# Performance work log

Hardware: AMD Instinct MI355X
Metric: run time of the kernel (lower is better)

The kernel has to match this reference:

```python
import jax, jax.numpy as jnp
import numpy as np
from jax import lax

E = 32          # num_experts
H = 1024        # hidden_size
I = 512         # expert intermediate_size
IS = 2048       # shared expert intermediate_size
G = 8           # n_group
TOPK_GROUP = 4
TOP_K = 8
SCALE = 2.5     # routed_scaling_factor
T = 1024        # tokens


def setup_inputs() -> dict:
    key = jax.random.key(0)
    ks = jax.random.split(key, 9)
    s = 0.02
    return {
        "hidden_states": jax.random.normal(ks[0], (T, H), jnp.float32),
        "gate_w": jax.random.normal(ks[1], (E, H), jnp.float32) * s,
        "e_bias": jax.random.normal(ks[2], (E,), jnp.float32) * 0.1,
        "w_gate": jax.random.normal(ks[3], (E, H, I), jnp.float32) * s,
        "w_up": jax.random.normal(ks[4], (E, H, I), jnp.float32) * s,
        "w_down": jax.random.normal(ks[5], (E, I, H), jnp.float32) * s,
        "ws_gate": jax.random.normal(ks[6], (H, IS), jnp.float32) * s,
        "ws_up": jax.random.normal(ks[7], (H, IS), jnp.float32) * s,
        "ws_down": jax.random.normal(ks[8], (IS, H), jnp.float32) * s,
    }


def _routing_combine(logits, e_bias):
    # Deepseekv3RoutingImpl.noaux_tc (non-fused reference path)
    scores = jax.nn.sigmoid(logits)                    # [T, E]
    swb = scores + e_bias                              # [T, E]
    swb_g = swb.reshape(-1, G, E // G)                 # [T, G, E/G]
    group_scores = lax.top_k(swb_g, 2)[0].sum(-1)      # sum of top-2 per group
    _, gidx = lax.top_k(group_scores, TOPK_GROUP)      # [T, TOPK_GROUP]
    gmask = jax.nn.one_hot(gidx, G, dtype=swb.dtype).sum(1)   # [T, G]
    smask = jnp.repeat(gmask, E // G, axis=-1)         # [T, E]
    _, tidx = lax.top_k(swb * smask, TOP_K)            # [T, TOP_K]
    emask = jax.nn.one_hot(tidx, E, dtype=scores.dtype).sum(1)
    sc = scores * emask
    combine = sc / (sc.sum(-1, keepdims=True) + 1e-20) * SCALE
    return combine, tidx


def reference(hidden_states, gate_w, e_bias, w_gate, w_up, w_down, ws_gate, ws_up, ws_down):
    x = hidden_states
    # gate: fp32 logits
    logits = x.astype(jnp.float32) @ gate_w.T          # [T, E]
    combine, _ = _routing_combine(logits, e_bias)
    # routed experts (FusedMoE math): per-expert gated MLP, combined by routing weights
    h1 = jnp.einsum('th,ehi->tei', x, w_gate)          # [T, E, I]
    h2 = jnp.einsum('th,ehi->tei', x, w_up)
    act = jax.nn.silu(h1) * h2
    routed = jnp.einsum('tei,te,eih->th', act, combine.astype(x.dtype), w_down)
    # shared expert GatedMLP
    shared = (jax.nn.silu(x @ ws_gate) * (x @ ws_up)) @ ws_down
    return routed + shared
```

## Files before the change

### kernel.cpp

```cpp
#include <hip/hip_runtime.h>
#include <cstdint>
#include <cmath>

#define T_TOK 1024
#define H_DIM 1024
#define E_NUM 32
#define I_DIM 512
#define IS_DIM 2048
#define NCOL_R 16384
#define NCOL_T 18432
#define SCALE_F 2.5f
#define MAXTILES 96

typedef __bf16 bf16x8 __attribute__((ext_vector_type(8)));
typedef float f32x4 __attribute__((ext_vector_type(4)));

typedef __attribute__((address_space(3))) unsigned int lds_u32_t;
typedef __attribute__((address_space(1))) const unsigned int glb_u32_t;

__device__ __forceinline__ unsigned short f2b(float f) {
    union { float f; uint32_t u; } v; v.f = f;
    return (unsigned short)((v.u + 0x7FFFu + ((v.u >> 16) & 1u)) >> 16);
}

__device__ __forceinline__ uint32_t cvt2(float lo, float hi) {
    uint32_t r;
    asm("v_cvt_pk_bf16_f32 %0, %1, %2" : "=v"(r) : "v"(lo), "v"(hi));
    return r;
}

__device__ __forceinline__ void gll16(const unsigned short* g, unsigned short* l) {
    __builtin_amdgcn_global_load_lds((glb_u32_t*)g, (lds_u32_t*)l, 16, 0, 0);
}

__device__ __forceinline__ void routing_wave(const float* __restrict__ x,
                                             const float* __restrict__ gate_w,
                                             const float* __restrict__ e_bias,
                                             float* __restrict__ combine,
                                             int* __restrict__ topk, int t) {
    int l = threadIdx.x & 63;
    int e = l & 31, half = l >> 5;
    const float4* xr = reinterpret_cast<const float4*>(x + (size_t)t * H_DIM + half * 512);
    const float4* wr = reinterpret_cast<const float4*>(gate_w + (size_t)e * H_DIM + half * 512);
    float s = 0.f;
#pragma unroll 8
    for (int j = 0; j < 128; j++) {
        float4 a = xr[j], b = wr[j];
        s += a.x * b.x + a.y * b.y + a.z * b.z + a.w * b.w;
    }
    s += __shfl_xor(s, 32);
    float sg = 1.f / (1.f + expf(-s));
    float swb = sg + e_bias[e];
    float v1 = __shfl_xor(swb, 1), v2 = __shfl_xor(swb, 2), v3 = __shfl_xor(swb, 3);
    float hi01 = fmaxf(swb, v1), lo01 = fminf(swb, v1);
    float hi23 = fmaxf(v2, v3),  lo23 = fminf(v2, v3);
    float gs = fmaxf(hi01, hi23) + fmaxf(fminf(hi01, hi23), fmaxf(lo01, lo23));
    int g = e >> 2;
    int grank = 0;
#pragma unroll
    for (int gg = 0; gg < 8; gg++) {
        float og = __shfl(gs, gg * 4);
        grank += ((og > gs) || (og == gs && gg < g)) ? 1 : 0;
    }
    bool gsel = grank < 4;
    float candv = gsel ? swb : 0.0f;
    int erank = 0;
#pragma unroll
    for (int ee = 0; ee < 32; ee++) {
        float oc = __shfl(candv, ee);
        erank += ((oc > candv) || (oc == candv && ee < e)) ? 1 : 0;
    }
    bool esel = (erank < 8) && (half == 0);
    unsigned long long m = __ballot(esel);
    int idx = __popcll(m & ((1ull << l) - 1ull));
    if (esel) topk[t * 8 + idx] = e;
    float r = esel ? sg : 0.f;
#pragma unroll
    for (int off = 1; off < 64; off <<= 1) r += __shfl_xor(r, off);
    float inv = SCALE_F / (r + 1e-20f);
    if (half == 0) combine[t * E_NUM + e] = esel ? sg * inv : 0.0f;
}

__global__ __launch_bounds__(256)
void prep1_kernel(const float* __restrict__ x, const float* __restrict__ gate_w,
                  const float* __restrict__ e_bias,
                  unsigned short* __restrict__ xb, float* __restrict__ combine,
                  int* __restrict__ topk) {
    int b = blockIdx.x;
    if (b < 256) {
        int t = b * 4 + (threadIdx.x >> 6);
        routing_wave(x, gate_w, e_bias, combine, topk, t);
        return;
    }
    int bb = b - 256;
#pragma unroll
    for (int p = 0; p < 4; p++) {
        int i = bb * 1024 + p * 256 + threadIdx.x;
        float4 v = reinterpret_cast<const float4*>(x)[i];
        uint2 o;
        o.x = cvt2(v.x, v.y);
        o.y = cvt2(v.z, v.w);
        reinterpret_cast<uint2*>(xb)[i] = o;
    }
}

__global__ __launch_bounds__(1024)
void listbuild_kernel(const int* __restrict__ topk, int* __restrict__ meta,
                      int* __restrict__ pair_token, int* __restrict__ slot_of) {
    __shared__ int cnt[E_NUM], start[E_NUM], fill[E_NUM];
    int t = threadIdx.x;
    if (t < E_NUM) cnt[t] = 0;
    __syncthreads();
    int ids[8];
#pragma unroll
    for (int r = 0; r < 8; r++) {
        ids[r] = topk[t * 8 + r];
        atomicAdd(&cnt[ids[r]], 1);
    }
    __syncthreads();
    if (t == 0) {
        int acc = 0;
        for (int e = 0; e < E_NUM; e++) {
            int nt = (cnt[e] + 127) >> 7;
            start[e] = acc * 128;
            fill[e] = 0;
            for (int j = 0; j < nt; j++) meta[1 + acc + j] = e;
            acc += nt;
        }
        meta[0] = acc;
    }
    __syncthreads();
    for (int i = t; i < MAXTILES * 128; i += 1024) pair_token[i] = 0;
    __syncthreads();
#pragma unroll
    for (int r = 0; r < 8; r++) {
        int e = ids[r];
        int s = start[e] + atomicAdd(&fill[e], 1);
        pair_token[s] = t;
        slot_of[t * 8 + r] = s;
    }
}

__global__ __launch_bounds__(256, 2)
void gateup_fused(const unsigned short* __restrict__ xb,
                  const float* __restrict__ w_gate,
                  const float* __restrict__ w_up,
                  const float* __restrict__ ws_gate,
                  const float* __restrict__ ws_up,
                  const float* __restrict__ combine,
                  const int* __restrict__ pair_token,
                  const int* __restrict__ meta,
                  unsigned short* __restrict__ act_s,
                  unsigned short* __restrict__ act_sh) {
    int b = blockIdx.x;
    bool routed = b < 384;
    int tid = threadIdx.x, lane = tid & 63, w = tid >> 6;
    int wr = w >> 1, wc = w & 1;
    __shared__ __align__(16) unsigned short lA[2][128 * 32];
    __shared__ __align__(16) unsigned short lBg[2][128 * 40];
    __shared__ __align__(16) unsigned short lBu[2][128 * 40];

    int srow = w * 32 + (lane >> 2);
    int schunk = (lane & 3) * 8;
    int aoff = (w * 32) * 32;

    const unsigned short *gA0, *gA1;
    const float *gBg, *gBu;
    int bstride;
    int e = 0, slot0 = 0, row0 = 0, ci0 = 0;
    if (routed) {
        int tile = b >> 2;
        if (tile >= meta[0]) return;
        e = meta[1 + tile];
        ci0 = (b & 3) * 128;
        slot0 = tile * 128;
        int tok0 = pair_token[slot0 + srow];
        int tok1 = pair_token[slot0 + srow + 16];
        gA0 = xb + (size_t)tok0 * H_DIM + schunk;
        gA1 = xb + (size_t)tok1 * H_DIM + schunk;
        gBg = w_gate + (size_t)e * H_DIM * I_DIM + ci0;
        gBu = w_up   + (size_t)e * H_DIM * I_DIM + ci0;
        bstride = I_DIM;
    } else {
        int bb = b - 384;
        row0 = (bb >> 4) * 128;
        ci0 = (bb & 15) * 128;
        gA0 = xb + (size_t)(row0 + srow) * H_DIM + schunk;
        gA1 = gA0 + 16 * H_DIM;
        gBg = ws_gate + ci0;
        gBu = ws_up + ci0;
        bstride = IS_DIM;
    }
    int bcol = tid & 127, khalf = tid >> 7;

    f32x4 accg[4][4], accu[4][4];
#pragma unroll
    for (int i = 0; i < 4; i++)
#pragma unroll
        for (int j = 0; j < 4; j++)
#pragma unroll
            for (int r = 0; r < 4; r++) { accg[i][j][r] = 0.f; accu[i][j][r] = 0.f; }

    float rg[16], ru[16];

#define GU_LOADB(KK)                                                    \
    do {                                                                \
        size_t kb = (size_t)((KK) * 32 + khalf * 16);                   \
        _Pragma("unroll")                                               \
        for (int j = 0; j < 16; j++) {                                  \
            rg[j] = gBg[(kb + j) * bstride + bcol];                     \
            ru[j] = gBu[(kb + j) * bstride + bcol];                     \
        }                                                               \
    } while (0)

#define GU_GLLA(KK, BSEL)                                               \
    do {                                                                \
        int _k0 = (KK) * 32;                                            \
        unsigned short* _a = &lA[BSEL][aoff];                           \
        gll16(gA0 + _k0, _a);                                           \
        gll16(gA1 + _k0, _a + 16 * 32);                                 \
    } while (0)

#define GU_WRB(BSEL)                                                    \
    do {                                                                \
        uint4 u;                                                        \
        unsigned short* dg = &lBg[BSEL][bcol * 40 + khalf * 16];        \
        u.x = cvt2(rg[0], rg[1]);  u.y = cvt2(rg[2], rg[3]);            \
        u.z = cvt2(rg[4], rg[5]);  u.w = cvt2(rg[6], rg[7]);            \
        *reinterpret_cast<uint4*>(dg) = u;                              \
        u.x = cvt2(rg[8], rg[9]);  u.y = cvt2(rg[10], rg[11]);          \
        u.z = cvt2(rg[12], rg[13]); u.w = cvt2(rg[14], rg[15]);         \
        *reinterpret_cast<uint4*>(dg + 8) = u;                          \
        unsigned short* du = &lBu[BSEL][bcol * 40 + khalf * 16];        \
        u.x = cvt2(ru[0], ru[1]);  u.y = cvt2(ru[2], ru[3]);            \
        u.z = cvt2(ru[4], ru[5]);  u.w = cvt2(ru[6], ru[7]);            \
        *reinterpret_cast<uint4*>(du) = u;                              \
        u.x = cvt2(ru[8], ru[9]);  u.y = cvt2(ru[10], ru[11]);          \
        u.z = cvt2(ru[12], ru[13]); u.w = cvt2(ru[14], ru[15]);         \
        *reinterpret_cast<uint4*>(du + 8) = u;                          \
    } while (0)

    GU_GLLA(0, 0);
    GU_LOADB(0);
    __syncthreads();
    GU_WRB(0);
    __syncthreads();
    for (int kk = 0; kk < 32; kk++) {
        int cur = kk & 1;
        if (kk < 31) { GU_GLLA(kk + 1, cur ^ 1); GU_LOADB(kk + 1); }
        bf16x8 af[4], bgf[4], buf2[4];
#pragma unroll
        for (int mi = 0; mi < 4; mi++)
            af[mi] = *reinterpret_cast<const bf16x8*>(
                &lA[cur][(wr * 64 + mi * 16 + (lane & 15)) * 32 + (lane >> 4) * 8]);
#pragma unroll
        for (int ni = 0; ni < 4; ni++) {
            int nn = (wc * 64 + ni * 16 + (lane & 15)) * 40 + (lane >> 4) * 8;
            bgf[ni] = *reinterpret_cast<const bf16x8*>(&lBg[cur][nn]);
            buf2[ni] = *reinterpret_cast<const bf16x8*>(&lBu[cur][nn]);
        }
#pragma unroll
        for (int mi = 0; mi < 4; mi++)
#pragma unroll
            for (int ni = 0; ni < 4; ni++) {
                accg[mi][ni] = __builtin_amdgcn_mfma_f32_16x16x32_bf16(af[mi], bgf[ni], accg[mi][ni], 0, 0, 0);
                accu[mi][ni] = __builtin_amdgcn_mfma_f32_16x16x32_bf16(af[mi], buf2[ni], accu[mi][ni], 0, 0, 0);
            }
        __syncthreads();
        if (kk < 31) {
            GU_WRB(cur ^ 1);
            __syncthreads();
        }
    }
#undef GU_LOADB
#undef GU_GLLA
#undef GU_WRB

    int q = lane >> 4, cl = lane & 15;
    if (routed) {
#pragma unroll
        for (int mi = 0; mi < 4; mi++) {
#pragma unroll
            for (int r = 0; r < 4; r++) {
                int row = wr * 64 + mi * 16 + q * 4 + r;
                int token = pair_token[slot0 + row];
                float s = combine[token * E_NUM + e];
#pragma unroll
                for (int ni = 0; ni < 4; ni++) {
                    float g = accg[mi][ni][r], u = accu[mi][ni][r];
                    float a = g / (1.f + expf(-g)) * u * s;
                    act_s[(size_t)(slot0 + row) * I_DIM + ci0 + wc * 64 + ni * 16 + cl] = f2b(a);
                }
            }
        }
    } else {
#pragma unroll
        for (int mi = 0; mi < 4; mi++) {
#pragma unroll
            for (int ni = 0; ni < 4; ni++) {
                int col = ci0 + wc * 64 + ni * 16 + cl;
#pragma unroll
                for (int r = 0; r < 4; r++) {
                    int row = row0 + wr * 64 + mi * 16 + q * 4 + r;
                    float g = accg[mi][ni][r], u = accu[mi][ni][r];
                    float a = g / (1.f + expf(-g)) * u;
                    act_sh[(size_t)row * IS_DIM + col] = f2b(a);
                }
            }
        }
    }
}

__global__ __launch_bounds__(256, 3)
void down_fused(const unsigned short* __restrict__ act_s,
                const float* __restrict__ w_down,
                const unsigned short* __restrict__ act_sh,
                const float* __restrict__ ws_down,
                const int* __restrict__ meta,
                float* __restrict__ pairpart,
                float* __restrict__ shpart) {
    int b = blockIdx.x;
    bool routed = b < 768;
    int tid = threadIdx.x, lane = tid & 63, w = tid >> 6;
    int wr = w >> 1, wc = w & 1;
    __shared__ __align__(16) unsigned short lA[2][128 * 32];
    __shared__ __align__(16) unsigned short lB[2][128 * 40];

    int srow = w * 32 + (lane >> 2);
    int schunk = (lane & 3) * 8;
    int aoff = (w * 32) * 32;

    const unsigned short* gA0;
    const float* gB;
    size_t ast;
    int kbase, n0, orow;
    float* outp;
    if (routed) {
        int tile = b >> 3;
        if (tile >= meta[0]) return;
        int e = meta[1 + tile];
        n0 = (b & 7) * 128;
        int slot0 = tile * 128;
        gA0 = act_s + (size_t)(slot0 + srow) * I_DIM + schunk;
        gB = w_down + (size_t)e * I_DIM * H_DIM + n0;
        ast = I_DIM; kbase = 0;
        outp = pairpart; orow = slot0;
    } else {
        int bb = b - 768;
        int mb = bb >> 5, nb = (bb >> 2) & 7, ks = bb & 3;
        int row0 = mb * 128;
        n0 = nb * 128;
        gA0 = act_sh + (size_t)(row0 + srow) * IS_DIM + schunk;
        gB = ws_down + n0;
        ast = IS_DIM; kbase = ks * 512;
        outp = shpart + ((size_t)ks << 20); orow = row0;
    }
    int bcol = tid & 127, khalf = tid >> 7;

    f32x4 acc[4][4];
#pragma unroll
    for (int i = 0; i < 4; i++)
#pragma unroll
        for (int j = 0; j < 4; j++)
#pragma unroll
            for (int r = 0; r < 4; r++) acc[i][j][r] = 0.f;

    float rb[16];

#define DN_LOADB(KK)                                                    \
    do {                                                                \
        size_t kb = (size_t)(kbase + (KK) * 32 + khalf * 16);           \
        _Pragma("unroll")                                               \
        for (int j = 0; j < 16; j++)                                    \
            rb[j] = gB[(kb + j) * H_DIM + bcol];                        \
    } while (0)

#define DN_GLLA(KK, BSEL)                                               \
    do {                                                                \
        size_t _k0 = (size_t)kbase + (size_t)(KK) * 32;                 \
        unsigned short* _a = &lA[BSEL][aoff];                           \
        gll16(gA0 + _k0, _a);                                           \
        gll16(gA0 + 16 * ast + _k0, _a + 16 * 32);                      \
    } while (0)

#define DN_WRB(BSEL)                                                    \
    do {                                                                \
        uint4 u;                                                        \
        unsigned short* d = &lB[BSEL][bcol * 40 + khalf * 16];          \
        u.x = cvt2(rb[0], rb[1]);  u.y = cvt2(rb[2], rb[3]);            \
        u.z = cvt2(rb[4], rb[5]);  u.w = cvt2(rb[6], rb[7]);            \
        *reinterpret_cast<uint4*>(d) = u;                               \
        u.x = cvt2(rb[8], rb[9]);  u.y = cvt2(rb[10], rb[11]);          \
        u.z = cvt2(rb[12], rb[13]); u.w = cvt2(rb[14], rb[15]);         \
        *reinterpret_cast<uint4*>(d + 8) = u;                           \
    } while (0)

    DN_GLLA(0, 0);
    DN_LOADB(0);
    __syncthreads();
    DN_WRB(0);
    __syncthreads();
    for (int kk = 0; kk < 16; kk++) {
        int cur = kk & 1;
        if (kk < 15) { DN_GLLA(kk + 1, cur ^ 1); DN_LOADB(kk + 1); }
        bf16x8 af[4], bf[4];
#pragma unroll
        for (int mi = 0; mi < 4; mi++)
            af[mi] = *reinterpret_cast<const bf16x8*>(
                &lA[cur][(wr * 64 + mi * 16 + (lane & 15)) * 32 + (lane >> 4) * 8]);
#pragma unroll
        for (int ni = 0; ni < 4; ni++)
            bf[ni] = *reinterpret_cast<const bf16x8*>(
                &lB[cur][(wc * 64 + ni * 16 + (lane & 15)) * 40 + (lane >> 4) * 8]);
#pragma unroll
        for (int mi = 0; mi < 4; mi++)
#pragma unroll
            for (int ni = 0; ni < 4; ni++)
                acc[mi][ni] = __builtin_amdgcn_mfma_f32_16x16x32_bf16(af[mi], bf[ni], acc[mi][ni], 0, 0, 0);
        __syncthreads();
        if (kk < 15) {
            DN_WRB(cur ^ 1);
            __syncthreads();
        }
    }
#undef DN_LOADB
#undef DN_GLLA
#undef DN_WRB

    int q = lane >> 4, cl = lane & 15;
#pragma unroll
    for (int mi = 0; mi < 4; mi++) {
#pragma unroll
        for (int ni = 0; ni < 4; ni++) {
            int col = n0 + wc * 64 + ni * 16 + cl;
#pragma unroll
            for (int r = 0; r < 4; r++) {
                int row = orow + wr * 64 + mi * 16 + q * 4 + r;
                outp[(size_t)row * H_DIM + col] = acc[mi][ni][r];
            }
        }
    }
}

__global__ void final_combine(const float* __restrict__ pairpart,
                              const float* __restrict__ shpart,
                              const int* __restrict__ slot_of,
                              float* __restrict__ out) {
    int t = blockIdx.x;
    int h = threadIdx.x * 4;
    float4 o = reinterpret_cast<const float4*>(shpart + (size_t)t * H_DIM + h)[0];
#pragma unroll
    for (int ks = 1; ks < 4; ks++) {
        float4 v = reinterpret_cast<const float4*>(shpart + ((size_t)ks << 20) + (size_t)t * H_DIM + h)[0];
        o.x += v.x; o.y += v.y; o.z += v.z; o.w += v.w;
    }
#pragma unroll
    for (int r = 0; r < 8; r++) {
        int s = slot_of[t * 8 + r];
        float4 v = reinterpret_cast<const float4*>(pairpart + (size_t)s * H_DIM + h)[0];
        o.x += v.x; o.y += v.y; o.z += v.z; o.w += v.w;
    }
    reinterpret_cast<float4*>(out + (size_t)t * H_DIM + h)[0] = o;
}


__global__ void cvt_x_kernel(const float* __restrict__ x, unsigned short* __restrict__ xb) {
    int i = blockIdx.x * 256 + threadIdx.x;
    float4 v = reinterpret_cast<const float4*>(x)[i];
    uint2 o;
    o.x = (uint32_t)f2b(v.x) | ((uint32_t)f2b(v.y) << 16);
    o.y = (uint32_t)f2b(v.z) | ((uint32_t)f2b(v.w) << 16);
    reinterpret_cast<uint2*>(xb)[i] = o;
}

__global__ void routing_kernel(const float* __restrict__ x,
                               const float* __restrict__ gate_w,
                               const float* __restrict__ e_bias,
                               float* __restrict__ combine,
                               int* __restrict__ topk) {
    int t = blockIdx.x;
    routing_wave(x, gate_w, e_bias, combine, topk, t);
}

__global__ __launch_bounds__(256, 2)
void gateup_kernel(const unsigned short* __restrict__ xb,
                   const float* __restrict__ w_gate,
                   const float* __restrict__ w_up,
                   const float* __restrict__ ws_gate,
                   const float* __restrict__ ws_up,
                   const float* __restrict__ combine,
                   unsigned short* __restrict__ act) {
    int mb = blockIdx.x, cb = blockIdx.y;
    int row0 = mb * 128, c0 = cb * 128;
    const float *bg, *bu;
    int bstride, eidx;
    if (c0 < NCOL_R) {
        int e = c0 >> 9, ci = c0 & 511;
        bg = w_gate + (size_t)e * H_DIM * I_DIM + ci;
        bu = w_up   + (size_t)e * H_DIM * I_DIM + ci;
        bstride = I_DIM; eidx = e;
    } else {
        int ci = c0 - NCOL_R;
        bg = ws_gate + ci; bu = ws_up + ci;
        bstride = IS_DIM; eidx = -1;
    }
    __shared__ __align__(16) unsigned short lA[128*32];
    __shared__ __align__(16) unsigned short lBg[128*32];
    __shared__ __align__(16) unsigned short lBu[128*32];
    int tid = threadIdx.x, lane = tid & 63, w = tid >> 6;
    int wr = w >> 1, wc = w & 1;
    f32x4 accg[4][4], accu[4][4];
#pragma unroll
    for (int i = 0; i < 4; i++)
#pragma unroll
        for (int j = 0; j < 4; j++)
#pragma unroll
            for (int r = 0; r < 4; r++) { accg[i][j][r] = 0.f; accu[i][j][r] = 0.f; }
    int ar = tid >> 2, ak = (tid & 3) * 8;
    int bn = tid & 127, bkg = (tid >> 7) * 16;
    for (int kk = 0; kk < H_DIM / 32; kk++) {
        int k0 = kk * 32;
        __syncthreads();
        *reinterpret_cast<uint4*>(&lA[ar*32 + ak]) =
            *reinterpret_cast<const uint4*>(xb + (size_t)(row0 + ar) * H_DIM + k0 + ak);
        *reinterpret_cast<uint4*>(&lA[(ar+64)*32 + ak]) =
            *reinterpret_cast<const uint4*>(xb + (size_t)(row0 + ar + 64) * H_DIM + k0 + ak);
#pragma unroll
        for (int p = 0; p < 4; p++) {
            int kb = bkg + p * 4;
            const float* pg = bg + (size_t)(k0 + kb) * bstride + bn;
            uint2 dg;
            dg.x = (uint32_t)f2b(pg[0])         | ((uint32_t)f2b(pg[bstride])   << 16);
            dg.y = (uint32_t)f2b(pg[2*bstride]) | ((uint32_t)f2b(pg[3*bstride]) << 16);
            *reinterpret_cast<uint2*>(&lBg[bn*32 + kb]) = dg;
            const float* pu = bu + (size_t)(k0 + kb) * bstride + bn;
            uint2 du;
            du.x = (uint32_t)f2b(pu[0])         | ((uint32_t)f2b(pu[bstride])   << 16);
            du.y = (uint32_t)f2b(pu[2*bstride]) | ((uint32_t)f2b(pu[3*bstride]) << 16);
            *reinterpret_cast<uint2*>(&lBu[bn*32 + kb]) = du;
        }
        __syncthreads();
        bf16x8 af[4], bgf[4], buf2[4];
#pragma unroll
        for (int mi = 0; mi < 4; mi++)
            af[mi] = *reinterpret_cast<const bf16x8*>(&lA[(wr*64 + mi*16 + (lane & 15))*32 + (lane >> 4)*8]);
#pragma unroll
        for (int ni = 0; ni < 4; ni++) {
            int nn = (wc*64 + ni*16 + (lane & 15))*32 + (lane >> 4)*8;
            bgf[ni]  = *reinterpret_cast<const bf16x8*>(&lBg[nn]);
            buf2[ni] = *reinterpret_cast<const bf16x8*>(&lBu[nn]);
        }
#pragma unroll
        for (int mi = 0; mi < 4; mi++)
#pragma unroll
            for (int ni = 0; ni < 4; ni++) {
                accg[mi][ni] = __builtin_amdgcn_mfma_f32_16x16x32_bf16(af[mi], bgf[ni],  accg[mi][ni], 0, 0, 0);
                accu[mi][ni] = __builtin_amdgcn_mfma_f32_16x16x32_bf16(af[mi], buf2[ni], accu[mi][ni], 0, 0, 0);
            }
    }
    int q = lane >> 4, cl = lane & 15;
#pragma unroll
    for (int mi = 0; mi < 4; mi++) {
#pragma unroll
        for (int ni = 0; ni < 4; ni++) {
            int colg = c0 + wc*64 + ni*16 + cl;
#pragma unroll
            for (int r = 0; r < 4; r++) {
                int row = row0 + wr*64 + mi*16 + q*4 + r;
                float g = accg[mi][ni][r], u = accu[mi][ni][r];
                float a = g / (1.f + expf(-g)) * u;
                float s = (eidx >= 0) ? combine[row * E_NUM + eidx] : 1.0f;
                act[(size_t)row * NCOL_T + colg] = f2b(a * s);
            }
        }
    }
}

__global__ __launch_bounds__(256, 2)
void down_kernel(const unsigned short* __restrict__ act,
                 const float* __restrict__ w_down,
                 const float* __restrict__ ws_down,
                 float* __restrict__ partials) {
    int mb = blockIdx.x, nb = blockIdx.y, ks = blockIdx.z;
    int row0 = mb * 128, n0 = nb * 128;
    __shared__ __align__(16) unsigned short lA[128*32];
    __shared__ __align__(16) unsigned short lB[128*32];
    int tid = threadIdx.x, lane = tid & 63, w = tid >> 6;
    int wr = w >> 1, wc = w & 1;
    f32x4 acc[4][4];
#pragma unroll
    for (int i = 0; i < 4; i++)
#pragma unroll
        for (int j = 0; j < 4; j++)
#pragma unroll
            for (int r = 0; r < 4; r++) acc[i][j][r] = 0.f;
    int ar = tid >> 2, ak = (tid & 3) * 8;
    int bn = tid & 127, bkg = (tid >> 7) * 16;
    for (int kk = 0; kk < 144; kk++) {
        int k0 = ks * 4608 + kk * 32;
        const float* bb = (k0 < NCOL_R) ? (w_down + (size_t)k0 * H_DIM)
                                        : (ws_down + (size_t)(k0 - NCOL_R) * H_DIM);
        __syncthreads();
        *reinterpret_cast<uint4*>(&lA[ar*32 + ak]) =
            *reinterpret_cast<const uint4*>(act + (size_t)(row0 + ar) * NCOL_T + k0 + ak);
        *reinterpret_cast<uint4*>(&lA[(ar+64)*32 + ak]) =
            *reinterpret_cast<const uint4*>(act + (size_t)(row0 + ar + 64) * NCOL_T + k0 + ak);
#pragma unroll
        for (int p = 0; p < 4; p++) {
            int kb = bkg + p * 4;
            const float* pb = bb + (size_t)kb * H_DIM + n0 + bn;
            uint2 d;
            d.x = (uint32_t)f2b(pb[0])       | ((uint32_t)f2b(pb[H_DIM])   << 16);
            d.y = (uint32_t)f2b(pb[2*H_DIM]) | ((uint32_t)f2b(pb[3*H_DIM]) << 16);
            *reinterpret_cast<uint2*>(&lB[bn*32 + kb]) = d;
        }
        __syncthreads();
        bf16x8 af[4], bf[4];
#pragma unroll
        for (int mi = 0; mi < 4; mi++)
            af[mi] = *reinterpret_cast<const bf16x8*>(&lA[(wr*64 + mi*16 + (lane & 15))*32 + (lane >> 4)*8]);
#pragma unroll
        for (int ni = 0; ni < 4; ni++)
            bf[ni] = *reinterpret_cast<const bf16x8*>(&lB[(wc*64 + ni*16 + (lane & 15))*32 + (lane >> 4)*8]);
#pragma unroll
        for (int mi = 0; mi < 4; mi++)
#pragma unroll
            for (int ni = 0; ni < 4; ni++)
                acc[mi][ni] = __builtin_amdgcn_mfma_f32_16x16x32_bf16(af[mi], bf[ni], acc[mi][ni], 0, 0, 0);
    }
    float* pout = partials + ((size_t)ks << 20);
    int q = lane >> 4, cl = lane & 15;
#pragma unroll
    for (int mi = 0; mi < 4; mi++) {
#pragma unroll
        for (int ni = 0; ni < 4; ni++) {
            int col = n0 + wc*64 + ni*16 + cl;
#pragma unroll
            for (int r = 0; r < 4; r++) {
                int row = row0 + wr*64 + mi*16 + q*4 + r;
                pout[(size_t)row * H_DIM + col] = acc[mi][ni][r];
            }
        }
    }
}

__global__ void reduce_kernel(const float* __restrict__ p, float* __restrict__ out) {
    int i = blockIdx.x * 256 + threadIdx.x;
    float4 a = reinterpret_cast<const float4*>(p)[i];
    float4 b = reinterpret_cast<const float4*>(p + (size_t)1048576)[i];
    float4 c = reinterpret_cast<const float4*>(p + (size_t)2097152)[i];
    float4 d = reinterpret_cast<const float4*>(p + (size_t)3145728)[i];
    float4 o;
    o.x = a.x + b.x + c.x + d.x;
    o.y = a.y + b.y + c.y + d.y;
    o.z = a.z + b.z + c.z + d.z;
    o.w = a.w + b.w + c.w + d.w;
    reinterpret_cast<float4*>(out)[i] = o;
}

extern "C" void kernel_launch(void* const* d_in, const int* in_sizes, int n_in,
                              void* d_out, int out_size, void* d_ws, size_t ws_size,
                              hipStream_t stream) {
    const float* x       = (const float*)d_in[0];
    const float* gate_w  = (const float*)d_in[1];
    const float* e_bias  = (const float*)d_in[2];
    const float* w_gate  = (const float*)d_in[3];
    const float* w_up    = (const float*)d_in[4];
    const float* w_down  = (const float*)d_in[5];
    const float* ws_gate = (const float*)d_in[6];
    const float* ws_up   = (const float*)d_in[7];
    const float* ws_down = (const float*)d_in[8];
    float* out = (float*)d_out;

    char* ws = (char*)d_ws;
    bool fast = ws_size >= 170000384ull;

    if (fast) {
        float* combine      = (float*)(ws);
        int*   topk         = (int*)(ws + 131072);
        int*   meta         = (int*)(ws + 163840);
        int*   pair_token   = (int*)(ws + 164352);
        int*   slot_of      = (int*)(ws + 213504);
        unsigned short* xb  = (unsigned short*)(ws + 262144);
        unsigned short* act_s  = (unsigned short*)(ws + 2359296);
        unsigned short* act_sh = (unsigned short*)(ws + 14942208);
        float* pairpart     = (float*)(ws + 19136512);
        float* shpart       = (float*)(ws + 69468160);

        prep1_kernel<<<512, 256, 0, stream>>>(x, gate_w, e_bias, xb, combine, topk);
        listbuild_kernel<<<1, 1024, 0, stream>>>(topk, meta, pair_token, slot_of);
        gateup_fused<<<512, 256, 0, stream>>>(xb, w_gate, w_up, ws_gate, ws_up,
                                              combine, pair_token, meta, act_s, act_sh);
        down_fused<<<1024, 256, 0, stream>>>(act_s, w_down, act_sh, ws_down, meta,
                                             pairpart, shpart);
        final_combine<<<1024, 256, 0, stream>>>(pairpart, shpart, slot_of, out);
    } else {
        float* combine     = (float*)(ws);
        int*   topk        = (int*)(ws + 131072);
        unsigned short* xb = (unsigned short*)(ws + 262144);
        unsigned short* act= (unsigned short*)(ws + 2359296);
        float* partials    = (float*)(ws + 40108032);

        cvt_x_kernel<<<1024, 256, 0, stream>>>(x, xb);
        routing_kernel<<<1024, 64, 0, stream>>>(x, gate_w, e_bias, combine, topk);
        gateup_kernel<<<dim3(8, 144), 256, 0, stream>>>(xb, w_gate, w_up, ws_gate, ws_up, combine, act);
        down_kernel<<<dim3(8, 8, 4), 256, 0, stream>>>(act, w_down, ws_down, partials);
        reduce_kernel<<<1024, 256, 0, stream>>>(partials, out);
    }
}
```

Measured before the change: 337.8 us.

## Halve gate/up column tile, single-buffer B in LDS, vectorize weight loads

The gate/up kernel's N tile drops from 128 to 64 columns, so the grid doubles to 1024 blocks and accumulator registers are halved. Occupancy hints rise to 4 blocks per CU in both GEMM kernels. The B-operand LDS buffers become single-buffered. Global fp32 weight loads become float2 reads, with each thread writing transposed bf16 pairs for two adjacent columns. The aim is more resident waves and fewer load instructions, at the cost of re-reading each A tile twice as often and less reuse per block.

```diff
diff --git a/kernel.cpp b/kernel.cpp
--- a/kernel.cpp
+++ b/kernel.cpp
@@ -141,7 +141,7 @@
     }
 }
 
-__global__ __launch_bounds__(256, 2)
+__global__ __launch_bounds__(256, 4)
 void gateup_fused(const unsigned short* __restrict__ xb,
                   const float* __restrict__ w_gate,
                   const float* __restrict__ w_up,
@@ -153,26 +153,28 @@
                   unsigned short* __restrict__ act_s,
                   unsigned short* __restrict__ act_sh) {
     int b = blockIdx.x;
-    bool routed = b < 384;
+    bool routed = b < 768;
     int tid = threadIdx.x, lane = tid & 63, w = tid >> 6;
     int wr = w >> 1, wc = w & 1;
     __shared__ __align__(16) unsigned short lA[2][128 * 32];
-    __shared__ __align__(16) unsigned short lBg[2][128 * 40];
-    __shared__ __align__(16) unsigned short lBu[2][128 * 40];
+    __shared__ __align__(16) unsigned short lBg[64 * 40];
+    __shared__ __align__(16) unsigned short lBu[64 * 40];
 
     int srow = w * 32 + (lane >> 2);
     int schunk = (lane & 3) * 8;
     int aoff = (w * 32) * 32;
+    int nc = (tid & 31) * 2;
+    int kg = tid >> 5;
 
     const unsigned short *gA0, *gA1;
     const float *gBg, *gBu;
     int bstride;
     int e = 0, slot0 = 0, row0 = 0, ci0 = 0;
     if (routed) {
-        int tile = b >> 2;
+        int tile = b >> 3;
         if (tile >= meta[0]) return;
         e = meta[1 + tile];
-        ci0 = (b & 3) * 128;
+        ci0 = (b & 7) * 64;
         slot0 = tile * 128;
         int tok0 = pair_token[slot0 + srow];
         int tok1 = pair_token[slot0 + srow + 16];
@@ -182,34 +184,33 @@
         gBu = w_up   + (size_t)e * H_DIM * I_DIM + ci0;
         bstride = I_DIM;
     } else {
-        int bb = b - 384;
-        row0 = (bb >> 4) * 128;
-        ci0 = (bb & 15) * 128;
+        int bb = b - 768;
+        row0 = (bb >> 5) * 128;
+        ci0 = (bb & 31) * 64;
         gA0 = xb + (size_t)(row0 + srow) * H_DIM + schunk;
         gA1 = gA0 + 16 * H_DIM;
         gBg = ws_gate + ci0;
         gBu = ws_up + ci0;
         bstride = IS_DIM;
     }
-    int bcol = tid & 127, khalf = tid >> 7;
-
-    f32x4 accg[4][4], accu[4][4];
+
+    f32x4 accg[4][2], accu[4][2];
 #pragma unroll
     for (int i = 0; i < 4; i++)
 #pragma unroll
-        for (int j = 0; j < 4; j++)
+        for (int j = 0; j < 2; j++)
 #pragma unroll
             for (int r = 0; r < 4; r++) { accg[i][j][r] = 0.f; accu[i][j][r] = 0.f; }
 
-    float rg[16], ru[16];
+    float2 vg[4], vu[4];
 
 #define GU_LOADB(KK)                                                    \
     do {                                                                \
-        size_t kb = (size_t)((KK) * 32 + khalf * 16);                   \
+        size_t kb = (size_t)((KK) * 32 + kg * 4);                       \
         _Pragma("unroll")                                               \
-        for (int j = 0; j < 16; j++) {                                  \
-            rg[j] = gBg[(kb + j) * bstride + bcol];                     \
-            ru[j] = gBu[(kb + j) * bstride + bcol];                     \
+        for (int j = 0; j < 4; j++) {                                   \
+            vg[j] = *reinterpret_cast<const float2*>(&gBg[(kb + j) * bstride + nc]); \
+            vu[j] = *reinterpret_cast<const float2*>(&gBu[(kb + j) * bstride + nc]); \
         }                                                               \
     } while (0)
 
@@ -221,54 +222,48 @@
         gll16(gA1 + _k0, _a + 16 * 32);                                 \
     } while (0)
 
-#define GU_WRB(BSEL)                                                    \
+#define GU_WRB()                                                        \
     do {                                                                \
-        uint4 u;                                                        \
-        unsigned short* dg = &lBg[BSEL][bcol * 40 + khalf * 16];        \
-        u.x = cvt2(rg[0], rg[1]);  u.y = cvt2(rg[2], rg[3]);            \
-        u.z = cvt2(rg[4], rg[5]);  u.w = cvt2(rg[6], rg[7]);            \
-        *reinterpret_cast<uint4*>(dg) = u;                              \
-        u.x = cvt2(rg[8], rg[9]);  u.y = cvt2(rg[10], rg[11]);          \
-        u.z = cvt2(rg[12], rg[13]); u.w = cvt2(rg[14], rg[15]);         \
-        *reinterpret_cast<uint4*>(dg + 8) = u;                          \
-        unsigned short* du = &lBu[BSEL][bcol * 40 + khalf * 16];        \
-        u.x = cvt2(ru[0], ru[1]);  u.y = cvt2(ru[2], ru[3]);            \
-        u.z = cvt2(ru[4], ru[5]);  u.w = cvt2(ru[6], ru[7]);            \
-        *reinterpret_cast<uint4*>(du) = u;                              \
-        u.x = cvt2(ru[8], ru[9]);  u.y = cvt2(ru[10], ru[11]);          \
-        u.z = cvt2(ru[12], ru[13]); u.w = cvt2(ru[14], ru[15]);         \
-        *reinterpret_cast<uint4*>(du + 8) = u;                          \
+        uint2 u;                                                        \
+        u.x = cvt2(vg[0].x, vg[1].x); u.y = cvt2(vg[2].x, vg[3].x);     \
+        *reinterpret_cast<uint2*>(&lBg[nc * 40 + kg * 4]) = u;          \
+        u.x = cvt2(vg[0].y, vg[1].y); u.y = cvt2(vg[2].y, vg[3].y);     \
+        *reinterpret_cast<uint2*>(&lBg[(nc + 1) * 40 + kg * 4]) = u;    \
+        u.x = cvt2(vu[0].x, vu[1].x); u.y = cvt2(vu[2].x, vu[3].x);     \
+        *reinterpret_cast<uint2*>(&lBu[nc * 40 + kg * 4]) = u;          \
+        u.x = cvt2(vu[0].y, vu[1].y); u.y = cvt2(vu[2].y, vu[3].y);     \
+        *reinterpret_cast<uint2*>(&lBu[(nc + 1) * 40 + kg * 4]) = u;    \
     } while (0)
 
     GU_GLLA(0, 0);
     GU_LOADB(0);
     __syncthreads();
-    GU_WRB(0);
+    GU_WRB();
     __syncthreads();
     for (int kk = 0; kk < 32; kk++) {
         int cur = kk & 1;
         if (kk < 31) { GU_GLLA(kk + 1, cur ^ 1); GU_LOADB(kk + 1); }
-        bf16x8 af[4], bgf[4], buf2[4];
+        bf16x8 af[4], bgf[2], buf2[2];
 #pragma unroll
         for (int mi = 0; mi < 4; mi++)
             af[mi] = *reinterpret_cast<const bf16x8*>(
                 &lA[cur][(wr * 64 + mi * 16 + (lane & 15)) * 32 + (lane >> 4) * 8]);
 #pragma unroll
-        for (int ni = 0; ni < 4; ni++) {
-            int nn = (wc * 64 + ni * 16 + (lane & 15)) * 40 + (lane >> 4) * 8;
-            bgf[ni] = *reinterpret_cast<const bf16x8*>(&lBg[cur][nn]);
-            buf2[ni] = *reinterpret_cast<const bf16x8*>(&lBu[cur][nn]);
+        for (int ni = 0; ni < 2; ni++) {
+            int nn = (wc * 32 + ni * 16 + (lane & 15)) * 40 + (lane >> 4) * 8;
+            bgf[ni] = *reinterpret_cast<const bf16x8*>(&lBg[nn]);
+            buf2[ni] = *reinterpret_cast<const bf16x8*>(&lBu[nn]);
         }
 #pragma unroll
         for (int mi = 0; mi < 4; mi++)
 #pragma unroll
-            for (int ni = 0; ni < 4; ni++) {
+            for (int ni = 0; ni < 2; ni++) {
                 accg[mi][ni] = __builtin_amdgcn_mfma_f32_16x16x32_bf16(af[mi], bgf[ni], accg[mi][ni], 0, 0, 0);
                 accu[mi][ni] = __builtin_amdgcn_mfma_f32_16x16x32_bf16(af[mi], buf2[ni], accu[mi][ni], 0, 0, 0);
             }
         __syncthreads();
         if (kk < 31) {
-            GU_WRB(cur ^ 1);
+            GU_WRB();
             __syncthreads();
         }
     }
@@ -286,10 +281,10 @@
                 int token = pair_token[slot0 + row];
                 float s = combine[token * E_NUM + e];
 #pragma unroll
-                for (int ni = 0; ni < 4; ni++) {
+                for (int ni = 0; ni < 2; ni++) {
                     float g = accg[mi][ni][r], u = accu[mi][ni][r];
                     float a = g / (1.f + expf(-g)) * u * s;
-                    act_s[(size_t)(slot0 + row) * I_DIM + ci0 + wc * 64 + ni * 16 + cl] = f2b(a);
+                    act_s[(size_t)(slot0 + row) * I_DIM + ci0 + wc * 32 + ni * 16 + cl] = f2b(a);
                 }
             }
         }
@@ -297,8 +292,8 @@
 #pragma unroll
         for (int mi = 0; mi < 4; mi++) {
 #pragma unroll
-            for (int ni = 0; ni < 4; ni++) {
-                int col = ci0 + wc * 64 + ni * 16 + cl;
+            for (int ni = 0; ni < 2; ni++) {
+                int col = ci0 + wc * 32 + ni * 16 + cl;
 #pragma unroll
                 for (int r = 0; r < 4; r++) {
                     int row = row0 + wr * 64 + mi * 16 + q * 4 + r;
@@ -311,7 +306,7 @@
     }
 }
 
-__global__ __launch_bounds__(256, 3)
+__global__ __launch_bounds__(256, 4)
 void down_fused(const unsigned short* __restrict__ act_s,
                 const float* __restrict__ w_down,
                 const unsigned short* __restrict__ act_sh,
@@ -324,11 +319,13 @@
     int tid = threadIdx.x, lane = tid & 63, w = tid >> 6;
     int wr = w >> 1, wc = w & 1;
     __shared__ __align__(16) unsigned short lA[2][128 * 32];
-    __shared__ __align__(16) unsigned short lB[2][128 * 40];
+    __shared__ __align__(16) unsigned short lB[128 * 40];
 
     int srow = w * 32 + (lane >> 2);
     int schunk = (lane & 3) * 8;
     int aoff = (w * 32) * 32;
+    int nc = (tid & 63) * 2;
+    int kg = tid >> 6;
 
     const unsigned short* gA0;
     const float* gB;
@@ -355,7 +352,6 @@
         ast = IS_DIM; kbase = ks * 512;
         outp = shpart + ((size_t)ks << 20); orow = row0;
     }
-    int bcol = tid & 127, khalf = tid >> 7;
 
     f32x4 acc[4][4];
 #pragma unroll
@@ -365,14 +361,14 @@
 #pragma unroll
             for (int r = 0; r < 4; r++) acc[i][j][r] = 0.f;
 
-    float rb[16];
+    float2 vb[8];
 
 #define DN_LOADB(KK)                                                    \
     do {                                                                \
-        size_t kb = (size_t)(kbase + (KK) * 32 + khalf * 16);           \
+        size_t kb = (size_t)(kbase + (KK) * 32 + kg * 8);               \
         _Pragma("unroll")                                               \
-        for (int j = 0; j < 16; j++)                                    \
-            rb[j] = gB[(kb + j) * H_DIM + bcol];                        \
+        for (int j = 0; j < 8; j++)                                     \
+            vb[j] = *reinterpret_cast<const float2*>(&gB[(kb + j) * H_DIM + nc]); \
     } while (0)
 
 #define DN_GLLA(KK, BSEL)                                               \
@@ -383,22 +379,21 @@
         gll16(gA0 + 16 * ast + _k0, _a + 16 * 32);                      \
     } while (0)
 
-#define DN_WRB(BSEL)                                                    \
+#define DN_WRB()                                                        \
     do {                                                                \
         uint4 u;                                                        \
-        unsigned short* d = &lB[BSEL][bcol * 40 + khalf * 16];          \
-        u.x = cvt2(rb[0], rb[1]);  u.y = cvt2(rb[2], rb[3]);            \
-        u.z = cvt2(rb[4], rb[5]);  u.w = cvt2(rb[6], rb[7]);            \
-        *reinterpret_cast<uint4*>(d) = u;                               \
-        u.x = cvt2(rb[8], rb[9]);  u.y = cvt2(rb[10], rb[11]);          \
-        u.z = cvt2(rb[12], rb[13]); u.w = cvt2(rb[14], rb[15]);         \
-        *reinterpret_cast<uint4*>(d + 8) = u;                           \
+        u.x = cvt2(vb[0].x, vb[1].x); u.y = cvt2(vb[2].x, vb[3].x);     \
+        u.z = cvt2(vb[4].x, vb[5].x); u.w = cvt2(vb[6].x, vb[7].x);     \
+        *reinterpret_cast<uint4*>(&lB[nc * 40 + kg * 8]) = u;           \
+        u.x = cvt2(vb[0].y, vb[1].y); u.y = cvt2(vb[2].y, vb[3].y);     \
+        u.z = cvt2(vb[4].y, vb[5].y); u.w = cvt2(vb[6].y, vb[7].y);     \
+        *reinterpret_cast<uint4*>(&lB[(nc + 1) * 40 + kg * 8]) = u;     \
     } while (0)
 
     DN_GLLA(0, 0);
     DN_LOADB(0);
     __syncthreads();
-    DN_WRB(0);
+    DN_WRB();
     __syncthreads();
     for (int kk = 0; kk < 16; kk++) {
         int cur = kk & 1;
@@ -411,7 +406,7 @@
 #pragma unroll
         for (int ni = 0; ni < 4; ni++)
             bf[ni] = *reinterpret_cast<const bf16x8*>(
-                &lB[cur][(wc * 64 + ni * 16 + (lane & 15)) * 40 + (lane >> 4) * 8]);
+                &lB[(wc * 64 + ni * 16 + (lane & 15)) * 40 + (lane >> 4) * 8]);
 #pragma unroll
         for (int mi = 0; mi < 4; mi++)
 #pragma unroll
@@ -419,7 +414,7 @@
                 acc[mi][ni] = __builtin_amdgcn_mfma_f32_16x16x32_bf16(af[mi], bf[ni], acc[mi][ni], 0, 0, 0);
         __syncthreads();
         if (kk < 15) {
-            DN_WRB(cur ^ 1);
+            DN_WRB();
             __syncthreads();
         }
     }
@@ -689,8 +684,8 @@
 
         prep1_kernel<<<512, 256, 0, stream>>>(x, gate_w, e_bias, xb, combine, topk);
         listbuild_kernel<<<1, 1024, 0, stream>>>(topk, meta, pair_token, slot_of);
-        gateup_fused<<<512, 256, 0, stream>>>(xb, w_gate, w_up, ws_gate, ws_up,
-                                              combine, pair_token, meta, act_s, act_sh);
+        gateup_fused<<<1024, 256, 0, stream>>>(xb, w_gate, w_up, ws_gate, ws_up,
+                                               combine, pair_token, meta, act_s, act_sh);
         down_fused<<<1024, 256, 0, stream>>>(act_s, w_down, act_sh, ws_down, meta,
                                              pairpart, shpart);
         final_combine<<<1024, 256, 0, stream>>>(pairpart, shpart, slot_of, out);
```

Measured after the change: 341.3 us. About the same (+1.0%).
